# Optimization experiments

Hardware: AMD Instinct MI355X
Metric: run time of the kernel (lower is better)

The kernel has to match this reference:

```python
import jax, jax.numpy as jnp
import numpy as np


def setup_inputs() -> dict:
    key = jax.random.key(0)
    ks = jax.random.split(key, 8)
    B, N, F = 16, 2048, 128
    x = jax.random.normal(ks[0], (B, N, F), dtype=jnp.float32)
    # dense (pre-normalized) adjacency, as spektral GCNConv expects normalized A
    a = jax.random.uniform(ks[1], (B, N, N), dtype=jnp.float32) / N
    w1 = jax.random.normal(ks[2], (F, 32), dtype=jnp.float32) * 0.1
    b1 = jnp.zeros((32,), dtype=jnp.float32)
    w2 = jax.random.normal(ks[3], (32, 32), dtype=jnp.float32) * 0.1
    b2 = jnp.zeros((32,), dtype=jnp.float32)
    wf1 = jax.random.normal(ks[4], (32, 512), dtype=jnp.float32) * 0.1
    bf1 = jnp.zeros((512,), dtype=jnp.float32)
    wf2 = jax.random.normal(ks[5], (512, 1), dtype=jnp.float32) * 0.1
    bf2 = jnp.zeros((1,), dtype=jnp.float32)
    return {"x": x, "a": a, "w1": w1, "b1": b1, "w2": w2, "b2": b2,
            "wf1": wf1, "bf1": bf1, "wf2": wf2, "bf2": bf2}


def _gcn(x, a, w, b):
    # GCNConv: elu(A_norm @ X @ W + b)
    h = jnp.einsum('bnf,fc->bnc', x, w)   # dense transform first (cheaper)
    h = jnp.einsum('bnm,bmc->bnc', a, h)  # adjacency aggregation
    return jax.nn.elu(h + b)


def reference(x, a, w1, b1, w2, b2, wf1, bf1, wf2, bf2):
    h = _gcn(x, a, w1, b1)                # [B,N,32]
    h = _gcn(h, a, w2, b2)                # [B,N,32]
    pooled = jnp.sum(h, axis=1)           # GlobalSumPool -> [B,32]
    h = jax.nn.relu(pooled @ wf1 + bf1)   # [B,512]
    out = jax.nn.sigmoid(h @ wf2 + bf2)   # [B,1]
    return out
```

## Files before the change

kernel.cpp:

```cpp
#include <hip/hip_runtime.h>
#include <hip/hip_bf16.h>
#include <math.h>

#define BATCH 16
#define NN 2048
#define FF 128
#define CC 32
#define HID 512

typedef float v4f __attribute__((ext_vector_type(4)));
typedef short short8 __attribute__((ext_vector_type(8)));

__device__ __forceinline__ unsigned short f2bf(float f) {
  unsigned u = __float_as_uint(f);
  u += 0x7fffu + ((u >> 16) & 1u);
  return (unsigned short)(u >> 16);
}

__device__ __forceinline__ float elu1(float x) {
  return x > 0.f ? x : expm1f(x);
}

__global__ __launch_bounds__(256)
void k_cvt(const float* __restrict__ a, unsigned short* __restrict__ abf) {
  long base = ((long)blockIdx.x * 256 + threadIdx.x) * 32;
  float4 f[8];
#pragma unroll
  for (int i = 0; i < 8; ++i) f[i] = *(const float4*)(a + base + i * 4);
#pragma unroll
  for (int i = 0; i < 4; ++i) {
    short8 r;
    r[0] = (short)f2bf(f[2 * i].x);     r[1] = (short)f2bf(f[2 * i].y);
    r[2] = (short)f2bf(f[2 * i].z);     r[3] = (short)f2bf(f[2 * i].w);
    r[4] = (short)f2bf(f[2 * i + 1].x); r[5] = (short)f2bf(f[2 * i + 1].y);
    r[6] = (short)f2bf(f[2 * i + 1].z); r[7] = (short)f2bf(f[2 * i + 1].w);
    *(short8*)(abf + base + i * 8) = r;
  }
}

__global__ __launch_bounds__(256)
void k_xw1(const float* __restrict__ src, const float* __restrict__ w,
           unsigned short* __restrict__ outT) {
  int t = threadIdx.x;
  int wv = t >> 6, l = t & 63, lo = l & 15, q = l >> 4;
  int rowt = blockIdx.x * 4 + wv;
  long row = (long)rowt * 16 + lo;

  short8 wf[FF / 32][2];
#pragma unroll
  for (int kc = 0; kc < FF / 32; ++kc)
#pragma unroll
    for (int h = 0; h < 2; ++h) {
      short8 f;
#pragma unroll
      for (int j = 0; j < 8; ++j)
        f[j] = (short)f2bf(w[(kc * 32 + q * 8 + j) * CC + h * 16 + lo]);
      wf[kc][h] = f;
    }

  v4f acc0 = {0.f, 0.f, 0.f, 0.f}, acc1 = {0.f, 0.f, 0.f, 0.f};
#pragma unroll
  for (int kc = 0; kc < FF / 32; ++kc) {
    const float* sp = src + row * FF + kc * 32 + q * 8;
    float4 a0 = *(const float4*)sp;
    float4 a1 = *(const float4*)(sp + 4);
    short8 af;
    af[0] = (short)f2bf(a0.x); af[1] = (short)f2bf(a0.y);
    af[2] = (short)f2bf(a0.z); af[3] = (short)f2bf(a0.w);
    af[4] = (short)f2bf(a1.x); af[5] = (short)f2bf(a1.y);
    af[6] = (short)f2bf(a1.z); af[7] = (short)f2bf(a1.w);
    acc0 = __builtin_amdgcn_mfma_f32_16x16x32_bf16(af, wf[kc][0], acc0, 0, 0, 0);
    acc1 = __builtin_amdgcn_mfma_f32_16x16x32_bf16(af, wf[kc][1], acc1, 0, 0, 0);
  }

  int b = rowt >> 7;
  int nbase = (rowt & 127) * 16;
#pragma unroll
  for (int r = 0; r < 4; ++r) {
    int n = nbase + q * 4 + r;
    outT[((long)b * CC + lo) * NN + n] = f2bf(acc0[r]);
    outT[((long)b * CC + 16 + lo) * NN + n] = f2bf(acc1[r]);
  }
}

__global__ __launch_bounds__(256)
void k_xw2(const float* __restrict__ h1f, const float* __restrict__ b1,
           const float* __restrict__ w2, unsigned short* __restrict__ outT) {
  const long HALF = (long)BATCH * NN * CC;
  int t = threadIdx.x;
  int wv = t >> 6, l = t & 63, lo = l & 15, q = l >> 4;
  int rowt = blockIdx.x * 4 + wv;
  long row = (long)rowt * 16 + lo;

  short8 wf[2];
#pragma unroll
  for (int h = 0; h < 2; ++h) {
    short8 f;
#pragma unroll
    for (int j = 0; j < 8; ++j)
      f[j] = (short)f2bf(w2[(q * 8 + j) * CC + h * 16 + lo]);
    wf[h] = f;
  }

  const float* p0 = h1f + row * CC + q * 8;
  const float* p1 = p0 + HALF;
  float4 x0 = *(const float4*)p0;
  float4 x1 = *(const float4*)(p0 + 4);
  float4 y0 = *(const float4*)p1;
  float4 y1 = *(const float4*)(p1 + 4);
  float bb[8];
#pragma unroll
  for (int j = 0; j < 8; ++j) bb[j] = b1[q * 8 + j];
  short8 af;
  af[0] = (short)f2bf(elu1(x0.x + y0.x + bb[0]));
  af[1] = (short)f2bf(elu1(x0.y + y0.y + bb[1]));
  af[2] = (short)f2bf(elu1(x0.z + y0.z + bb[2]));
  af[3] = (short)f2bf(elu1(x0.w + y0.w + bb[3]));
  af[4] = (short)f2bf(elu1(x1.x + y1.x + bb[4]));
  af[5] = (short)f2bf(elu1(x1.y + y1.y + bb[5]));
  af[6] = (short)f2bf(elu1(x1.z + y1.z + bb[6]));
  af[7] = (short)f2bf(elu1(x1.w + y1.w + bb[7]));

  v4f acc0 = {0.f, 0.f, 0.f, 0.f}, acc1 = {0.f, 0.f, 0.f, 0.f};
  acc0 = __builtin_amdgcn_mfma_f32_16x16x32_bf16(af, wf[0], acc0, 0, 0, 0);
  acc1 = __builtin_amdgcn_mfma_f32_16x16x32_bf16(af, wf[1], acc1, 0, 0, 0);

  int b = rowt >> 7;
  int nbase = (rowt & 127) * 16;
#pragma unroll
  for (int r = 0; r < 4; ++r) {
    int n = nbase + q * 4 + r;
    outT[((long)b * CC + lo) * NN + n] = f2bf(acc0[r]);
    outT[((long)b * CC + 16 + lo) * NN + n] = f2bf(acc1[r]);
  }
}

#define LSTR 1032

__global__ __launch_bounds__(256, 2)
void k_agg(const unsigned short* __restrict__ abf,
           const unsigned short* __restrict__ hT,
           float* __restrict__ hpart) {
  __shared__ unsigned short hs[CC * LSTR];

  int t = threadIdx.x;
  int bid = blockIdx.x;
  int rt = bid & 31, half = (bid >> 5) & 1, b = bid >> 6;

#pragma unroll
  for (int i = 0; i < 16; ++i) {
    int j = i * 256 + t;
    int c = j >> 7, off = (j & 127) * 8;
    uint4 v = *(const uint4*)(hT + ((long)b * CC + c) * NN + half * 1024 + off);
    *(uint4*)&hs[c * LSTR + off] = v;
  }
  __syncthreads();

  int wv = t >> 6, l = t & 63, lo = l & 15, q = l >> 4;
  int n0 = rt * 64 + wv * 16;
  const unsigned short* arow =
      abf + ((long)(b * NN + n0 + lo)) * NN + half * 1024 + q * 8;
  const unsigned short* h0 = &hs[lo * LSTR + q * 8];

  v4f acc0 = {0.f, 0.f, 0.f, 0.f}, acc1 = {0.f, 0.f, 0.f, 0.f};
#pragma unroll
  for (int mm = 0; mm < 1024; mm += 32) {
    short8 af = *(const short8*)(arow + mm);
    short8 b0 = *(const short8*)(h0 + mm);
    short8 b1 = *(const short8*)(h0 + 16 * LSTR + mm);
    acc0 = __builtin_amdgcn_mfma_f32_16x16x32_bf16(af, b0, acc0, 0, 0, 0);
    acc1 = __builtin_amdgcn_mfma_f32_16x16x32_bf16(af, b1, acc1, 0, 0, 0);
  }

  float* op = hpart + ((long)half * BATCH * NN + (long)b * NN) * CC;
#pragma unroll
  for (int r = 0; r < 4; ++r) {
    int n = n0 + q * 4 + r;
    op[(long)n * CC + lo] = acc0[r];
    op[(long)n * CC + 16 + lo] = acc1[r];
  }
}

__global__ __launch_bounds__(256)
void k_pool(const float* __restrict__ h2f, const float* __restrict__ b2,
            float* __restrict__ pooled) {
  const long HALF = (long)BATCH * NN * CC;
  __shared__ float red[8][CC + 1];
  int t = threadIdx.x;
  int b = blockIdx.x >> 3, seg = blockIdx.x & 7;
  int c = t & 31, nl = t >> 5;
  float bc = b2[c];
  float s = 0.f;
  for (int n = seg * 256 + nl; n < seg * 256 + 256; n += 8) {
    long idx = ((long)b * NN + n) * CC + c;
    s += elu1(h2f[idx] + h2f[HALF + idx] + bc);
  }
  red[nl][c] = s;
  __syncthreads();
  if (nl < 4) red[nl][c] += red[nl + 4][c];
  __syncthreads();
  if (nl < 2) red[nl][c] += red[nl + 2][c];
  __syncthreads();
  if (nl == 0) atomicAdd(&pooled[b * CC + c], red[0][c] + red[1][c]);
}

__global__ __launch_bounds__(512)
void k5_mlp(const float* __restrict__ pooled, const float* __restrict__ wf1,
            const float* __restrict__ bf1, const float* __restrict__ wf2,
            const float* __restrict__ bf2, float* __restrict__ out) {
  __shared__ float red[HID];
  __shared__ float ps[CC];
  int b = blockIdx.x, j = threadIdx.x;
  if (j < CC) ps[j] = pooled[b * CC + j];
  __syncthreads();
  float acc = bf1[j];
#pragma unroll
  for (int c = 0; c < CC; ++c) acc += ps[c] * wf1[c * HID + j];
  red[j] = fmaxf(acc, 0.f) * wf2[j];
  __syncthreads();
  for (int s = HID / 2; s > 0; s >>= 1) {
    if (j < s) red[j] += red[j + s];
    __syncthreads();
  }
  if (j == 0) out[b] = 1.f / (1.f + expf(-(red[0] + bf2[0])));
}

extern "C" void kernel_launch(void* const* d_in, const int* in_sizes, int n_in,
                              void* d_out, int out_size, void* d_ws, size_t ws_size,
                              hipStream_t stream) {
  const float* x   = (const float*)d_in[0];
  const float* a   = (const float*)d_in[1];
  const float* w1  = (const float*)d_in[2];
  const float* b1  = (const float*)d_in[3];
  const float* w2  = (const float*)d_in[4];
  const float* b2  = (const float*)d_in[5];
  const float* wf1 = (const float*)d_in[6];
  const float* bf1 = (const float*)d_in[7];
  const float* wf2 = (const float*)d_in[8];
  const float* bf2 = (const float*)d_in[9];
  float* out = (float*)d_out;

  char* ws = (char*)d_ws;
  unsigned short* abf = (unsigned short*)ws;
  unsigned short* hT1 = (unsigned short*)(ws + 0x8000000UL);
  unsigned short* hT2 = (unsigned short*)(ws + 0x8200000UL);
  float* h1f = (float*)(ws + 0x8400000UL);
  float* h2f = (float*)(ws + 0x8C00000UL);
  float* pooled = (float*)(ws + 0x9400000UL);

  hipMemsetAsync(pooled, 0, BATCH * CC * sizeof(float), stream);

  k_cvt<<<8192, 256, 0, stream>>>(a, abf);
  k_xw1<<<512, 256, 0, stream>>>(x, w1, hT1);
  k_agg<<<1024, 256, 0, stream>>>(abf, hT1, h1f);
  k_xw2<<<512, 256, 0, stream>>>(h1f, b1, w2, hT2);
  k_agg<<<1024, 256, 0, stream>>>(abf, hT2, h2f);
  k_pool<<<128, 256, 0, stream>>>(h2f, b2, pooled);
  k5_mlp<<<BATCH, HID, 0, stream>>>(pooled, wf1, bf1, wf2, bf2, out);
}
```

Baseline: 483.8 us.

## Fuse fp32-to-bf16 adjacency conversion into first aggregation and split K into quarters

Removes the standalone conversion kernel: the first aggregation reads fp32 A directly, converts to bf16 in registers, feeds MFMA, and writes the bf16 copy for the second layer. The K dimension is split into four 512-wide chunks instead of two, doubling grid size and halving shared memory per block to allow more resident blocks. This saves one full read of the fp32 adjacency and a kernel launch, at the cost of four partial-sum buffers that downstream kernels must sum.

```diff
diff --git a/kernel.cpp b/kernel.cpp
--- a/kernel.cpp
+++ b/kernel.cpp
@@ -7,6 +7,8 @@
 #define FF 128
 #define CC 32
 #define HID 512
+#define QM 512
+#define LSTR 520
 
 typedef float v4f __attribute__((ext_vector_type(4)));
 typedef short short8 __attribute__((ext_vector_type(8)));
@@ -19,23 +21,6 @@
 
 __device__ __forceinline__ float elu1(float x) {
   return x > 0.f ? x : expm1f(x);
-}
-
-__global__ __launch_bounds__(256)
-void k_cvt(const float* __restrict__ a, unsigned short* __restrict__ abf) {
-  long base = ((long)blockIdx.x * 256 + threadIdx.x) * 32;
-  float4 f[8];
-#pragma unroll
-  for (int i = 0; i < 8; ++i) f[i] = *(const float4*)(a + base + i * 4);
-#pragma unroll
-  for (int i = 0; i < 4; ++i) {
-    short8 r;
-    r[0] = (short)f2bf(f[2 * i].x);     r[1] = (short)f2bf(f[2 * i].y);
-    r[2] = (short)f2bf(f[2 * i].z);     r[3] = (short)f2bf(f[2 * i].w);
-    r[4] = (short)f2bf(f[2 * i + 1].x); r[5] = (short)f2bf(f[2 * i + 1].y);
-    r[6] = (short)f2bf(f[2 * i + 1].z); r[7] = (short)f2bf(f[2 * i + 1].w);
-    *(short8*)(abf + base + i * 8) = r;
-  }
 }
 
 __global__ __launch_bounds__(256)
@@ -83,75 +68,74 @@
   }
 }
 
-__global__ __launch_bounds__(256)
-void k_xw2(const float* __restrict__ h1f, const float* __restrict__ b1,
-           const float* __restrict__ w2, unsigned short* __restrict__ outT) {
-  const long HALF = (long)BATCH * NN * CC;
-  int t = threadIdx.x;
-  int wv = t >> 6, l = t & 63, lo = l & 15, q = l >> 4;
-  int rowt = blockIdx.x * 4 + wv;
-  long row = (long)rowt * 16 + lo;
-
-  short8 wf[2];
-#pragma unroll
-  for (int h = 0; h < 2; ++h) {
-    short8 f;
-#pragma unroll
-    for (int j = 0; j < 8; ++j)
-      f[j] = (short)f2bf(w2[(q * 8 + j) * CC + h * 16 + lo]);
-    wf[h] = f;
-  }
-
-  const float* p0 = h1f + row * CC + q * 8;
-  const float* p1 = p0 + HALF;
-  float4 x0 = *(const float4*)p0;
-  float4 x1 = *(const float4*)(p0 + 4);
-  float4 y0 = *(const float4*)p1;
-  float4 y1 = *(const float4*)(p1 + 4);
-  float bb[8];
-#pragma unroll
-  for (int j = 0; j < 8; ++j) bb[j] = b1[q * 8 + j];
-  short8 af;
-  af[0] = (short)f2bf(elu1(x0.x + y0.x + bb[0]));
-  af[1] = (short)f2bf(elu1(x0.y + y0.y + bb[1]));
-  af[2] = (short)f2bf(elu1(x0.z + y0.z + bb[2]));
-  af[3] = (short)f2bf(elu1(x0.w + y0.w + bb[3]));
-  af[4] = (short)f2bf(elu1(x1.x + y1.x + bb[4]));
-  af[5] = (short)f2bf(elu1(x1.y + y1.y + bb[5]));
-  af[6] = (short)f2bf(elu1(x1.z + y1.z + bb[6]));
-  af[7] = (short)f2bf(elu1(x1.w + y1.w + bb[7]));
-
-  v4f acc0 = {0.f, 0.f, 0.f, 0.f}, acc1 = {0.f, 0.f, 0.f, 0.f};
-  acc0 = __builtin_amdgcn_mfma_f32_16x16x32_bf16(af, wf[0], acc0, 0, 0, 0);
-  acc1 = __builtin_amdgcn_mfma_f32_16x16x32_bf16(af, wf[1], acc1, 0, 0, 0);
-
-  int b = rowt >> 7;
-  int nbase = (rowt & 127) * 16;
-#pragma unroll
-  for (int r = 0; r < 4; ++r) {
-    int n = nbase + q * 4 + r;
-    outT[((long)b * CC + lo) * NN + n] = f2bf(acc0[r]);
-    outT[((long)b * CC + 16 + lo) * NN + n] = f2bf(acc1[r]);
-  }
-}
-
-#define LSTR 1032
-
-__global__ __launch_bounds__(256, 2)
-void k_agg(const unsigned short* __restrict__ abf,
-           const unsigned short* __restrict__ hT,
-           float* __restrict__ hpart) {
+__global__ __launch_bounds__(256, 4)
+void k_agg1(const float* __restrict__ a,
+            unsigned short* __restrict__ abf,
+            const unsigned short* __restrict__ hT,
+            float* __restrict__ hpart) {
   __shared__ unsigned short hs[CC * LSTR];
 
   int t = threadIdx.x;
   int bid = blockIdx.x;
-  int rt = bid & 31, half = (bid >> 5) & 1, b = bid >> 6;
-
-#pragma unroll
-  for (int i = 0; i < 16; ++i) {
+  int rt = bid & 31, qm = (bid >> 5) & 3, b = bid >> 7;
+
+#pragma unroll
+  for (int i = 0; i < 8; ++i) {
     int j = i * 256 + t;
-    int c = j >> 7, off = (j & 127) * 8;
-    uint4 v = *(const uint4*)(hT + ((long)b * CC + c) * NN + half * 1024 + off);
+    int c = j >> 6, off = (j & 63) * 8;
+    uint4 v = *(const uint4*)(hT + ((long)b * CC + c) * NN + qm * QM + off);
+    *(uint4*)&hs[c * LSTR + off] = v;
+  }
+  __syncthreads();
+
+  int wv = t >> 6, l = t & 63, lo = l & 15, q = l >> 4;
+  int n0 = rt * 64 + wv * 16;
+  long abase = ((long)(b * NN + n0 + lo)) * NN + qm * QM + q * 8;
+  const float* arow = a + abase;
+  unsigned short* aout = abf + abase;
+  const unsigned short* h0 = &hs[lo * LSTR + q * 8];
+
+  v4f acc0 = {0.f, 0.f, 0.f, 0.f}, acc1 = {0.f, 0.f, 0.f, 0.f};
+#pragma unroll
+  for (int mm = 0; mm < QM; mm += 32) {
+    float4 a0 = *(const float4*)(arow + mm);
+    float4 a1 = *(const float4*)(arow + mm + 4);
+    short8 af;
+    af[0] = (short)f2bf(a0.x); af[1] = (short)f2bf(a0.y);
+    af[2] = (short)f2bf(a0.z); af[3] = (short)f2bf(a0.w);
+    af[4] = (short)f2bf(a1.x); af[5] = (short)f2bf(a1.y);
+    af[6] = (short)f2bf(a1.z); af[7] = (short)f2bf(a1.w);
+    *(short8*)(aout + mm) = af;
+    short8 b0 = *(const short8*)(h0 + mm);
+    short8 b1 = *(const short8*)(h0 + 16 * LSTR + mm);
+    acc0 = __builtin_amdgcn_mfma_f32_16x16x32_bf16(af, b0, acc0, 0, 0, 0);
+    acc1 = __builtin_amdgcn_mfma_f32_16x16x32_bf16(af, b1, acc1, 0, 0, 0);
+  }
+
+  float* op = hpart + ((long)qm * BATCH * NN + (long)b * NN) * CC;
+#pragma unroll
+  for (int r = 0; r < 4; ++r) {
+    int n = n0 + q * 4 + r;
+    op[(long)n * CC + lo] = acc0[r];
+    op[(long)n * CC + 16 + lo] = acc1[r];
+  }
+}
+
+__global__ __launch_bounds__(256, 4)
+void k_agg2(const unsigned short* __restrict__ abf,
+            const unsigned short* __restrict__ hT,
+            float* __restrict__ hpart) {
+  __shared__ unsigned short hs[CC * LSTR];
+
+  int t = threadIdx.x;
+  int bid = blockIdx.x;
+  int rt = bid & 31, qm = (bid >> 5) & 3, b = bid >> 7;
+
+#pragma unroll
+  for (int i = 0; i < 8; ++i) {
+    int j = i * 256 + t;
+    int c = j >> 6, off = (j & 63) * 8;
+    uint4 v = *(const uint4*)(hT + ((long)b * CC + c) * NN + qm * QM + off);
     *(uint4*)&hs[c * LSTR + off] = v;
   }
   __syncthreads();
@@ -159,12 +143,12 @@
   int wv = t >> 6, l = t & 63, lo = l & 15, q = l >> 4;
   int n0 = rt * 64 + wv * 16;
   const unsigned short* arow =
-      abf + ((long)(b * NN + n0 + lo)) * NN + half * 1024 + q * 8;
+      abf + ((long)(b * NN + n0 + lo)) * NN + qm * QM + q * 8;
   const unsigned short* h0 = &hs[lo * LSTR + q * 8];
 
   v4f acc0 = {0.f, 0.f, 0.f, 0.f}, acc1 = {0.f, 0.f, 0.f, 0.f};
 #pragma unroll
-  for (int mm = 0; mm < 1024; mm += 32) {
+  for (int mm = 0; mm < QM; mm += 32) {
     short8 af = *(const short8*)(arow + mm);
     short8 b0 = *(const short8*)(h0 + mm);
     short8 b1 = *(const short8*)(h0 + 16 * LSTR + mm);
@@ -172,7 +156,7 @@
     acc1 = __builtin_amdgcn_mfma_f32_16x16x32_bf16(af, b1, acc1, 0, 0, 0);
   }
 
-  float* op = hpart + ((long)half * BATCH * NN + (long)b * NN) * CC;
+  float* op = hpart + ((long)qm * BATCH * NN + (long)b * NN) * CC;
 #pragma unroll
   for (int r = 0; r < 4; ++r) {
     int n = n0 + q * 4 + r;
@@ -182,9 +166,56 @@
 }
 
 __global__ __launch_bounds__(256)
-void k_pool(const float* __restrict__ h2f, const float* __restrict__ b2,
+void k_xw2(const float* __restrict__ h1p, const float* __restrict__ b1,
+           const float* __restrict__ w2, unsigned short* __restrict__ outT) {
+  const long QS = (long)BATCH * NN * CC;
+  int t = threadIdx.x;
+  int wv = t >> 6, l = t & 63, lo = l & 15, q = l >> 4;
+  int rowt = blockIdx.x * 4 + wv;
+  long row = (long)rowt * 16 + lo;
+
+  short8 wf[2];
+#pragma unroll
+  for (int h = 0; h < 2; ++h) {
+    short8 f;
+#pragma unroll
+    for (int j = 0; j < 8; ++j)
+      f[j] = (short)f2bf(w2[(q * 8 + j) * CC + h * 16 + lo]);
+    wf[h] = f;
+  }
+
+  const float* p = h1p + row * CC + q * 8;
+  float s[8] = {0, 0, 0, 0, 0, 0, 0, 0};
+#pragma unroll
+  for (int qq = 0; qq < 4; ++qq) {
+    float4 u0 = *(const float4*)(p + qq * QS);
+    float4 u1 = *(const float4*)(p + qq * QS + 4);
+    s[0] += u0.x; s[1] += u0.y; s[2] += u0.z; s[3] += u0.w;
+    s[4] += u1.x; s[5] += u1.y; s[6] += u1.z; s[7] += u1.w;
+  }
+  short8 af;
+#pragma unroll
+  for (int j = 0; j < 8; ++j)
+    af[j] = (short)f2bf(elu1(s[j] + b1[q * 8 + j]));
+
+  v4f acc0 = {0.f, 0.f, 0.f, 0.f}, acc1 = {0.f, 0.f, 0.f, 0.f};
+  acc0 = __builtin_amdgcn_mfma_f32_16x16x32_bf16(af, wf[0], acc0, 0, 0, 0);
+  acc1 = __builtin_amdgcn_mfma_f32_16x16x32_bf16(af, wf[1], acc1, 0, 0, 0);
+
+  int b = rowt >> 7;
+  int nbase = (rowt & 127) * 16;
+#pragma unroll
+  for (int r = 0; r < 4; ++r) {
+    int n = nbase + q * 4 + r;
+    outT[((long)b * CC + lo) * NN + n] = f2bf(acc0[r]);
+    outT[((long)b * CC + 16 + lo) * NN + n] = f2bf(acc1[r]);
+  }
+}
+
+__global__ __launch_bounds__(256)
+void k_pool(const float* __restrict__ h2p, const float* __restrict__ b2,
             float* __restrict__ pooled) {
-  const long HALF = (long)BATCH * NN * CC;
+  const long QS = (long)BATCH * NN * CC;
   __shared__ float red[8][CC + 1];
   int t = threadIdx.x;
   int b = blockIdx.x >> 3, seg = blockIdx.x & 7;
@@ -193,7 +224,7 @@
   float s = 0.f;
   for (int n = seg * 256 + nl; n < seg * 256 + 256; n += 8) {
     long idx = ((long)b * NN + n) * CC + c;
-    s += elu1(h2f[idx] + h2f[HALF + idx] + bc);
+    s += elu1(h2p[idx] + h2p[QS + idx] + h2p[2 * QS + idx] + h2p[3 * QS + idx] + bc);
   }
   red[nl][c] = s;
   __syncthreads();
@@ -244,17 +275,16 @@
   unsigned short* abf = (unsigned short*)ws;
   unsigned short* hT1 = (unsigned short*)(ws + 0x8000000UL);
   unsigned short* hT2 = (unsigned short*)(ws + 0x8200000UL);
-  float* h1f = (float*)(ws + 0x8400000UL);
-  float* h2f = (float*)(ws + 0x8C00000UL);
-  float* pooled = (float*)(ws + 0x9400000UL);
+  float* h1p = (float*)(ws + 0x8400000UL);
+  float* h2p = (float*)(ws + 0x9400000UL);
+  float* pooled = (float*)(ws + 0xA400000UL);
 
   hipMemsetAsync(pooled, 0, BATCH * CC * sizeof(float), stream);
 
-  k_cvt<<<8192, 256, 0, stream>>>(a, abf);
   k_xw1<<<512, 256, 0, stream>>>(x, w1, hT1);
-  k_agg<<<1024, 256, 0, stream>>>(abf, hT1, h1f);
-  k_xw2<<<512, 256, 0, stream>>>(h1f, b1, w2, hT2);
-  k_agg<<<1024, 256, 0, stream>>>(abf, hT2, h2f);
-  k_pool<<<128, 256, 0, stream>>>(h2f, b2, pooled);
+  k_agg1<<<2048, 256, 0, stream>>>(a, abf, hT1, h1p);
+  k_xw2<<<512, 256, 0, stream>>>(h1p, b1, w2, hT2);
+  k_agg2<<<2048, 256, 0, stream>>>(abf, hT2, h2p);
+  k_pool<<<128, 256, 0, stream>>>(h2p, b2, pooled);
   k5_mlp<<<BATCH, HID, 0, stream>>>(pooled, wf1, bf1, wf2, bf2, out);
 }
```

Result: faster. 460.4 us (-4.8%).
